# Performance work log

Measured on AMD Instinct MI355X. Metric: run time of the kernel, lower is better.

Reference implementation:

```python
import jax, jax.numpy as jnp
import numpy as np

D = 128

def setup_inputs() -> dict:
    key = jax.random.key(0)
    ks = jax.random.split(key, 9)
    B, Nq, Nk = 4, 4096, 4096
    Q = jax.random.normal(ks[0], (B, Nq, D), dtype=jnp.float32)
    K = jax.random.normal(ks[1], (B, Nk, D), dtype=jnp.float32)
    V = jax.random.normal(ks[2], (B, Nk, D), dtype=jnp.float32)
    s = 1.0 / np.sqrt(D)
    Wq = jax.random.normal(ks[3], (D, D), dtype=jnp.float32) * s
    Wk = jax.random.normal(ks[4], (D, D), dtype=jnp.float32) * s
    Wv = jax.random.normal(ks[5], (D, D), dtype=jnp.float32) * s
    bq = jax.random.normal(ks[6], (D,), dtype=jnp.float32) * s
    bk = jax.random.normal(ks[7], (D,), dtype=jnp.float32) * s
    bv = jax.random.normal(ks[8], (D,), dtype=jnp.float32) * s
    return {"Q": Q, "K": K, "V": V, "Wq": Wq, "bq": bq, "Wk": Wk, "bk": bk, "Wv": Wv, "bv": bv}

def reference(Q, K, V, Wq, bq, Wk, bk, Wv, bv):
    scale = jnp.asarray(D ** 0.5, dtype=Q.dtype)
    # torch Linear: x @ W.T + b
    q = jnp.einsum('bnd,ed->bne', Q, Wq) + bq
    k = jnp.einsum('bnd,ed->bne', K, Wk) + bk
    v = jnp.einsum('bnd,ed->bne', V, Wv) + bv
    scores = jnp.einsum('bqe,bke->bqk', q, k) / scale  # [B, Nq, Nk]
    attn = jax.nn.softmax(scores, axis=-1)
    return jnp.einsum('bqk,bke->bqe', attn, v)
```

## Files before the change

kernel.cpp:

```cpp
#include <hip/hip_runtime.h>
#include <math.h>

#define D 128
#define NSPLIT 4

typedef __bf16 v8bf __attribute__((ext_vector_type(8)));
typedef __bf16 v4bf __attribute__((ext_vector_type(4)));
typedef float v4f __attribute__((ext_vector_type(4)));

__device__ inline v8bf load_cvt8(const float* __restrict__ p) {
  const float4* p4 = (const float4*)p;
  float4 a = p4[0], b = p4[1];
  v8bf r;
  r[0] = (__bf16)a.x; r[1] = (__bf16)a.y; r[2] = (__bf16)a.z; r[3] = (__bf16)a.w;
  r[4] = (__bf16)b.x; r[5] = (__bf16)b.y; r[6] = (__bf16)b.z; r[7] = (__bf16)b.w;
  return r;
}

__device__ inline void async_copy16(const void* gsrc, void* ldst) {
  __builtin_amdgcn_global_load_lds(
      (const __attribute__((address_space(1))) void*)gsrc,
      (__attribute__((address_space(3))) void*)ldst, 16, 0, 0);
}

__global__ __launch_bounds__(256) void proj_all(
    const float* __restrict__ Q, const float* __restrict__ K,
    const float* __restrict__ V,
    const float* __restrict__ Wq, const float* __restrict__ bq,
    const float* __restrict__ Wk, const float* __restrict__ bk,
    const float* __restrict__ Wv, const float* __restrict__ bv,
    __bf16* __restrict__ qbf, __bf16* __restrict__ kbf,
    __bf16* __restrict__ vtbf, int Nk, float alpha)
{
  __shared__ __align__(16) __bf16 w_lds[128][136];

  const float* W    = (blockIdx.y == 0) ? Wq : (blockIdx.y == 1) ? Wk : Wv;
  const float* bias = (blockIdx.y == 0) ? bq : (blockIdx.y == 1) ? bk : bv;

  {
    const int tid = threadIdx.x;
    const int r = tid >> 1;
    const int h = (tid & 1) * 64;
    #pragma unroll
    for (int i = 0; i < 8; ++i) {
      v8bf v = load_cvt8(W + r * D + h + i * 8);
      *(v8bf*)&w_lds[r][h + i * 8] = v;
    }
  }
  __syncthreads();

  const int w = threadIdx.x >> 6, l = threadIdx.x & 63;
  const int l16 = l & 15, l4 = l >> 4;

  if (blockIdx.y < 2) {
    const float* X = (blockIdx.y == 0) ? Q : K;
    __bf16* Y      = (blockIdx.y == 0) ? qbf : kbf;
    const float a  = (blockIdx.y == 0) ? alpha : 1.0f;
    const size_t rbase = (size_t)blockIdx.x * 64 + w * 16;

    v4f acc[8];
    #pragma unroll
    for (int ct = 0; ct < 8; ++ct) acc[ct] = (v4f){0.f, 0.f, 0.f, 0.f};

    #pragma unroll
    for (int kk = 0; kk < 4; ++kk) {
      v8bf xv = load_cvt8(X + (rbase + l16) * D + kk * 32 + l4 * 8);
      #pragma unroll
      for (int ct = 0; ct < 8; ++ct) {
        v8bf wv = *(const v8bf*)&w_lds[ct * 16 + l16][kk * 32 + l4 * 8];
        acc[ct] = __builtin_amdgcn_mfma_f32_16x16x32_bf16(wv, xv, acc[ct], 0, 0, 0);
      }
    }
    const size_t qrow = rbase + l16;
    #pragma unroll
    for (int ct = 0; ct < 8; ++ct) {
      const int e0 = ct * 16 + l4 * 4;
      float4 b4 = *(const float4*)(bias + e0);
      v4bf o;
      o[0] = (__bf16)((acc[ct][0] + b4.x) * a);
      o[1] = (__bf16)((acc[ct][1] + b4.y) * a);
      o[2] = (__bf16)((acc[ct][2] + b4.z) * a);
      o[3] = (__bf16)((acc[ct][3] + b4.w) * a);
      *(v4bf*)(Y + qrow * D + e0) = o;
    }
  } else {
    const int bx = blockIdx.x;
    const int b = bx >> 6;
    const float* Xb = V + (size_t)b * Nk * D;
    __bf16* VTb = vtbf + (size_t)b * D * Nk;
    const int ebase = w * 32;
    const int nbase = (bx & 63) * 64;

    v4f acc[4][2];
    #pragma unroll
    for (int nt = 0; nt < 4; ++nt)
      #pragma unroll
      for (int et = 0; et < 2; ++et) acc[nt][et] = (v4f){0.f, 0.f, 0.f, 0.f};

    #pragma unroll
    for (int kk = 0; kk < 4; ++kk) {
      v8bf wv0 = *(const v8bf*)&w_lds[ebase + l16][kk * 32 + l4 * 8];
      v8bf wv1 = *(const v8bf*)&w_lds[ebase + 16 + l16][kk * 32 + l4 * 8];
      #pragma unroll
      for (int nt = 0; nt < 4; ++nt) {
        v8bf xv = load_cvt8(Xb + (size_t)(nbase + nt * 16 + l16) * D + kk * 32 + l4 * 8);
        acc[nt][0] = __builtin_amdgcn_mfma_f32_16x16x32_bf16(xv, wv0, acc[nt][0], 0, 0, 0);
        acc[nt][1] = __builtin_amdgcn_mfma_f32_16x16x32_bf16(xv, wv1, acc[nt][1], 0, 0, 0);
      }
    }
    #pragma unroll
    for (int et = 0; et < 2; ++et) {
      const int e = ebase + et * 16 + l16;
      const float bv2 = bias[e];
      __bf16* dst = VTb + (size_t)e * Nk + nbase;
      #pragma unroll
      for (int nt = 0; nt < 4; ++nt) {
        v4bf o;
        o[0] = (__bf16)(acc[nt][et][0] + bv2);
        o[1] = (__bf16)(acc[nt][et][1] + bv2);
        o[2] = (__bf16)(acc[nt][et][2] + bv2);
        o[3] = (__bf16)(acc[nt][et][3] + bv2);
        *(v4bf*)(dst + nt * 16 + l4 * 4) = o;
      }
    }
  }
}

__global__ __launch_bounds__(512, 2) void attn_fwd(
    const __bf16* __restrict__ Qb, const __bf16* __restrict__ Kb,
    const __bf16* __restrict__ VTb, float* __restrict__ Out,
    float2* __restrict__ ml, int Nq, int Nk, int NS, int B)
{
  const int nwg = gridDim.x;
  int id = blockIdx.x;
  id = (id & 7) * (nwg >> 3) + (id >> 3);
  const int nx = Nq >> 7;
  const int x = id % nx;
  const int s = (id / nx) % NS;
  const int b = id / (nx * NS);

  const int w = threadIdx.x >> 6, l = threadIdx.x & 63;
  const int l16 = l & 15, l4 = l >> 4;
  const int qbase = x * 128 + w * 16;
  const int chunk = Nk / NS;
  const int kvbeg = s * chunk;
  const int ntiles = chunk >> 6;

  const __bf16* q = Qb + ((size_t)b * Nq + qbase) * D;
  const char* kg0 = (const char*)(Kb + (size_t)b * Nk * D);
  const char* vg0 = (const char*)(VTb + (size_t)b * D * Nk);

  __shared__ __align__(16) char k_lds[2][16384];
  __shared__ __align__(16) char v_lds[2][16384];
  __shared__ __align__(16) char p_lds[8 * 2048];
  char* my_p = p_lds + w * 2048;

  const int NkB = Nk * 2;

  v8bf aq[4];
  #pragma unroll
  for (int kk = 0; kk < 4; ++kk)
    aq[kk] = *(const v8bf*)(q + l16 * D + kk * 32 + l4 * 8);

  v4f accO[8];
  #pragma unroll
  for (int ct = 0; ct < 8; ++ct) accO[ct] = (v4f){0.f, 0.f, 0.f, 0.f};
  float m[4], lsum[4];
  #pragma unroll
  for (int r = 0; r < 4; ++r) { m[r] = -1e30f; lsum[r] = 0.f; }

  auto stage = [&](int kv0, int buf) {
    const char* kg = kg0 + (size_t)kv0 * (D * 2);
    #pragma unroll
    for (int sweep = 0; sweep < 2; ++sweep) {
      const int flat = sweep * 8192 + w * 1024 + l * 16;
      const int row = flat >> 8;
      const int c = flat & 255;
      async_copy16(kg + ((row << 8) | (c ^ ((row & 7) << 4))),
                   &k_lds[buf][sweep * 8192 + w * 1024]);
    }
    const char* vg = vg0 + (size_t)kv0 * 2;
    #pragma unroll
    for (int sweep = 0; sweep < 2; ++sweep) {
      const int flat = sweep * 8192 + w * 1024 + l * 16;
      const int row = flat >> 7;
      const int c = flat & 127;
      async_copy16(vg + (size_t)row * NkB + (c ^ ((row & 7) << 4)),
                   &v_lds[buf][sweep * 8192 + w * 1024]);
    }
  };

  stage(kvbeg, 0);
  __syncthreads();

  for (int t = 0; t < ntiles; ++t) {
    const int cur = t & 1;
    if (t + 1 < ntiles) stage(kvbeg + (t + 1) * 64, cur ^ 1);

    v4f sc4[4];
    #pragma unroll
    for (int ct = 0; ct < 4; ++ct) sc4[ct] = (v4f){0.f, 0.f, 0.f, 0.f};
    #pragma unroll
    for (int ct = 0; ct < 4; ++ct) {
      const int krow = ct * 16 + l16;
      const int sw = (krow & 7) << 4;
      #pragma unroll
      for (int kk = 0; kk < 4; ++kk) {
        const int cb = kk * 64 + l4 * 16;
        v8bf bk = *(const v8bf*)(&k_lds[cur][krow * 256 + (cb ^ sw)]);
        sc4[ct] = __builtin_amdgcn_mfma_f32_16x16x32_bf16(aq[kk], bk, sc4[ct], 0, 0, 0);
      }
    }

    float lmax[4];
    float g = -1e30f;
    #pragma unroll
    for (int r = 0; r < 4; ++r) {
      lmax[r] = fmaxf(fmaxf(sc4[0][r], sc4[1][r]), fmaxf(sc4[2][r], sc4[3][r]));
      g = fmaxf(g, lmax[r] - m[r]);
    }
    if (__all(g <= 8.0f)) {
      #pragma unroll
      for (int r = 0; r < 4; ++r) {
        float rs = 0.f;
        #pragma unroll
        for (int ct = 0; ct < 4; ++ct) {
          float p = exp2f(sc4[ct][r] - m[r]);
          sc4[ct][r] = p;
          rs += p;
        }
        lsum[r] += rs;
      }
    } else {
      float scale[4];
      #pragma unroll
      for (int r = 0; r < 4; ++r) {
        float mx = lmax[r];
        #pragma unroll
        for (int off = 8; off; off >>= 1) mx = fmaxf(mx, __shfl_xor(mx, off, 64));
        float mn = fmaxf(m[r], mx);
        scale[r] = exp2f(m[r] - mn);
        m[r] = mn;
        float rs = 0.f;
        #pragma unroll
        for (int ct = 0; ct < 4; ++ct) {
          float p = exp2f(sc4[ct][r] - mn);
          sc4[ct][r] = p;
          rs += p;
        }
        lsum[r] = lsum[r] * scale[r] + rs;
      }
      #pragma unroll
      for (int ct = 0; ct < 8; ++ct)
        #pragma unroll
        for (int r = 0; r < 4; ++r) accO[ct][r] *= scale[r];
    }

    #pragma unroll
    for (int ct = 0; ct < 4; ++ct)
      #pragma unroll
      for (int r = 0; r < 4; ++r) {
        const int row = l4 * 4 + r;
        const int byte = row * 128 + ((ct * 32 + l16 * 2) ^ ((row & 7) << 4));
        *(__bf16*)(my_p + byte) = (__bf16)sc4[ct][r];
      }

    #pragma unroll
    for (int ks = 0; ks < 2; ++ks) {
      const int cbp = ks * 64 + l4 * 16;
      v8bf ap = *(const v8bf*)(my_p + l16 * 128 + (cbp ^ ((l16 & 7) << 4)));
      #pragma unroll
      for (int ct = 0; ct < 8; ++ct) {
        const int vrow = ct * 16 + l16;
        const int cb = ks * 64 + l4 * 16;
        v8bf bv = *(const v8bf*)(&v_lds[cur][vrow * 128 + (cb ^ ((vrow & 7) << 4))]);
        accO[ct] = __builtin_amdgcn_mfma_f32_16x16x32_bf16(ap, bv, accO[ct], 0, 0, 0);
      }
    }
    __syncthreads();
  }

  #pragma unroll
  for (int r = 0; r < 4; ++r) {
    float t2 = lsum[r];
    #pragma unroll
    for (int off = 8; off; off >>= 1) t2 += __shfl_xor(t2, off, 64);
    lsum[r] = t2;
  }

  float* outp = Out + (((size_t)s * B + b) * Nq + qbase) * D;
  if (NS == 1) {
    #pragma unroll
    for (int ct = 0; ct < 8; ++ct)
      #pragma unroll
      for (int r = 0; r < 4; ++r)
        outp[(size_t)(l4 * 4 + r) * D + ct * 16 + l16] = accO[ct][r] / lsum[r];
  } else {
    #pragma unroll
    for (int ct = 0; ct < 8; ++ct)
      #pragma unroll
      for (int r = 0; r < 4; ++r)
        outp[(size_t)(l4 * 4 + r) * D + ct * 16 + l16] = accO[ct][r];
    if (l16 == 0) {
      #pragma unroll
      for (int r = 0; r < 4; ++r) {
        size_t row = (size_t)b * Nq + qbase + l4 * 4 + r;
        ml[(size_t)s * B * Nq + row] = make_float2(m[r], lsum[r]);
      }
    }
  }
}

__global__ __launch_bounds__(256) void attn_combine(
    const float* __restrict__ Opart, const float2* __restrict__ ml,
    float* __restrict__ out, int NS, int rowsTotal)
{
  const int t = threadIdx.x;
  const size_t row = (size_t)blockIdx.x * 2 + (t >> 7);
  const int d = t & 127;

  float mv[NSPLIT], lv[NSPLIT];
  float M = -1e30f;
  #pragma unroll
  for (int s = 0; s < NSPLIT; ++s) {
    float2 x = ml[(size_t)s * rowsTotal + row];
    mv[s] = x.x; lv[s] = x.y;
    M = fmaxf(M, x.x);
  }
  float denom = 0.f, acc = 0.f;
  #pragma unroll
  for (int s = 0; s < NSPLIT; ++s) {
    float wgt = exp2f(mv[s] - M);
    denom += wgt * lv[s];
    acc += wgt * Opart[((size_t)s * rowsTotal + row) * D + d];
  }
  out[row * D + d] = acc / denom;
}

extern "C" void kernel_launch(void* const* d_in, const int* in_sizes, int n_in,
                              void* d_out, int out_size, void* d_ws, size_t ws_size,
                              hipStream_t stream) {
  const float* Q  = (const float*)d_in[0];
  const float* K  = (const float*)d_in[1];
  const float* V  = (const float*)d_in[2];
  const float* Wq = (const float*)d_in[3];
  const float* bq = (const float*)d_in[4];
  const float* Wk = (const float*)d_in[5];
  const float* bk = (const float*)d_in[6];
  const float* Wv = (const float*)d_in[7];
  const float* bv = (const float*)d_in[8];
  float* out = (float*)d_out;

  const int B = 4, Nq = 4096, Nk = 4096;
  const size_t nElems = (size_t)B * Nq * D;
  const size_t bfBytes = nElems * 2;

  char* ws = (char*)d_ws;
  __bf16* qbf  = (__bf16*)(ws);
  __bf16* kbf  = (__bf16*)(ws + bfBytes);
  __bf16* vtbf = (__bf16*)(ws + 2 * bfBytes);
  float*  Opart = (float*)(ws + 3 * bfBytes);
  float2* mlp   = (float2*)(ws + 3 * bfBytes + (size_t)NSPLIT * nElems * 4);

  const size_t needSplit = 3 * bfBytes + (size_t)NSPLIT * nElems * 4 +
                           (size_t)NSPLIT * B * Nq * 8;
  const int NS = (ws_size >= needSplit) ? NSPLIT : 1;

  const float alpha = 1.4426950408889634f / sqrtf((float)D);

  proj_all<<<dim3(B * Nq / 64, 3), 256, 0, stream>>>(
      Q, K, V, Wq, bq, Wk, bk, Wv, bv, qbf, kbf, vtbf, Nk, alpha);

  const int nx = Nq / 128;
  if (NS == 1) {
    attn_fwd<<<dim3(nx * B), 512, 0, stream>>>(
        qbf, kbf, vtbf, out, nullptr, Nq, Nk, 1, B);
  } else {
    attn_fwd<<<dim3(nx * NS * B), 512, 0, stream>>>(
        qbf, kbf, vtbf, Opart, mlp, Nq, Nk, NS, B);
    attn_combine<<<dim3(B * Nq / 2), 256, 0, stream>>>(
        Opart, mlp, out, NS, B * Nq);
  }
}
```

Baseline: 181.4 us.

## Process 32 query rows per wave with 4 waves per block

Each wave now handles two 16-row query sub-tiles instead of one, so every K and V fragment read from LDS feeds two MFMAs. Blocks shrink from 8 waves to 4, with each wave issuing twice as many async copies for staging. This halves LDS read traffic per MFMA, at the cost of roughly doubled accumulator and score register use per wave, which may lower occupancy and cuts the number of waves available to hide latency.

```diff
diff --git a/kernel.cpp b/kernel.cpp
--- a/kernel.cpp
+++ b/kernel.cpp
@@ -126,7 +126,7 @@
   }
 }
 
-__global__ __launch_bounds__(512, 2) void attn_fwd(
+__global__ __launch_bounds__(256, 2) void attn_fwd(
     const __bf16* __restrict__ Qb, const __bf16* __restrict__ Kb,
     const __bf16* __restrict__ VTb, float* __restrict__ Out,
     float2* __restrict__ ml, int Nq, int Nk, int NS, int B)
@@ -141,7 +141,7 @@
 
   const int w = threadIdx.x >> 6, l = threadIdx.x & 63;
   const int l16 = l & 15, l4 = l >> 4;
-  const int qbase = x * 128 + w * 16;
+  const int qbase = x * 128 + w * 32;
   const int chunk = Nk / NS;
   const int kvbeg = s * chunk;
   const int ntiles = chunk >> 6;
@@ -152,41 +152,47 @@
 
   __shared__ __align__(16) char k_lds[2][16384];
   __shared__ __align__(16) char v_lds[2][16384];
-  __shared__ __align__(16) char p_lds[8 * 2048];
-  char* my_p = p_lds + w * 2048;
+  __shared__ __align__(16) char p_lds[4 * 4096];
+  char* my_p = p_lds + w * 4096;
 
   const int NkB = Nk * 2;
 
-  v8bf aq[4];
-  #pragma unroll
-  for (int kk = 0; kk < 4; ++kk)
-    aq[kk] = *(const v8bf*)(q + l16 * D + kk * 32 + l4 * 8);
-
-  v4f accO[8];
-  #pragma unroll
-  for (int ct = 0; ct < 8; ++ct) accO[ct] = (v4f){0.f, 0.f, 0.f, 0.f};
-  float m[4], lsum[4];
-  #pragma unroll
-  for (int r = 0; r < 4; ++r) { m[r] = -1e30f; lsum[r] = 0.f; }
+  v8bf aq[2][4];
+  #pragma unroll
+  for (int qs = 0; qs < 2; ++qs)
+    #pragma unroll
+    for (int kk = 0; kk < 4; ++kk)
+      aq[qs][kk] = *(const v8bf*)(q + (qs * 16 + l16) * D + kk * 32 + l4 * 8);
+
+  v4f accO[2][8];
+  #pragma unroll
+  for (int qs = 0; qs < 2; ++qs)
+    #pragma unroll
+    for (int ct = 0; ct < 8; ++ct) accO[qs][ct] = (v4f){0.f, 0.f, 0.f, 0.f};
+  float m[2][4], lsum[2][4];
+  #pragma unroll
+  for (int qs = 0; qs < 2; ++qs)
+    #pragma unroll
+    for (int r = 0; r < 4; ++r) { m[qs][r] = -1e30f; lsum[qs][r] = 0.f; }
 
   auto stage = [&](int kv0, int buf) {
     const char* kg = kg0 + (size_t)kv0 * (D * 2);
     #pragma unroll
-    for (int sweep = 0; sweep < 2; ++sweep) {
-      const int flat = sweep * 8192 + w * 1024 + l * 16;
+    for (int sweep = 0; sweep < 4; ++sweep) {
+      const int flat = sweep * 4096 + w * 1024 + l * 16;
       const int row = flat >> 8;
       const int c = flat & 255;
       async_copy16(kg + ((row << 8) | (c ^ ((row & 7) << 4))),
-                   &k_lds[buf][sweep * 8192 + w * 1024]);
+                   &k_lds[buf][sweep * 4096 + w * 1024]);
     }
     const char* vg = vg0 + (size_t)kv0 * 2;
     #pragma unroll
-    for (int sweep = 0; sweep < 2; ++sweep) {
-      const int flat = sweep * 8192 + w * 1024 + l * 16;
+    for (int sweep = 0; sweep < 4; ++sweep) {
+      const int flat = sweep * 4096 + w * 1024 + l * 16;
       const int row = flat >> 7;
       const int c = flat & 127;
       async_copy16(vg + (size_t)row * NkB + (c ^ ((row & 7) << 4)),
-                   &v_lds[buf][sweep * 8192 + w * 1024]);
+                   &v_lds[buf][sweep * 4096 + w * 1024]);
     }
   };
 
@@ -197,9 +203,11 @@
     const int cur = t & 1;
     if (t + 1 < ntiles) stage(kvbeg + (t + 1) * 64, cur ^ 1);
 
-    v4f sc4[4];
-    #pragma unroll
-    for (int ct = 0; ct < 4; ++ct) sc4[ct] = (v4f){0.f, 0.f, 0.f, 0.f};
+    v4f sc4[2][4];
+    #pragma unroll
+    for (int qs = 0; qs < 2; ++qs)
+      #pragma unroll
+      for (int ct = 0; ct < 4; ++ct) sc4[qs][ct] = (v4f){0.f, 0.f, 0.f, 0.f};
     #pragma unroll
     for (int ct = 0; ct < 4; ++ct) {
       const int krow = ct * 16 + l16;
@@ -208,105 +216,122 @@
       for (int kk = 0; kk < 4; ++kk) {
         const int cb = kk * 64 + l4 * 16;
         v8bf bk = *(const v8bf*)(&k_lds[cur][krow * 256 + (cb ^ sw)]);
-        sc4[ct] = __builtin_amdgcn_mfma_f32_16x16x32_bf16(aq[kk], bk, sc4[ct], 0, 0, 0);
-      }
-    }
-
-    float lmax[4];
-    float g = -1e30f;
-    #pragma unroll
-    for (int r = 0; r < 4; ++r) {
-      lmax[r] = fmaxf(fmaxf(sc4[0][r], sc4[1][r]), fmaxf(sc4[2][r], sc4[3][r]));
-      g = fmaxf(g, lmax[r] - m[r]);
-    }
-    if (__all(g <= 8.0f)) {
+        sc4[0][ct] = __builtin_amdgcn_mfma_f32_16x16x32_bf16(aq[0][kk], bk, sc4[0][ct], 0, 0, 0);
+        sc4[1][ct] = __builtin_amdgcn_mfma_f32_16x16x32_bf16(aq[1][kk], bk, sc4[1][ct], 0, 0, 0);
+      }
+    }
+
+    #pragma unroll
+    for (int qs = 0; qs < 2; ++qs) {
+      float lmax[4];
+      float g = -1e30f;
       #pragma unroll
       for (int r = 0; r < 4; ++r) {
-        float rs = 0.f;
-        #pragma unroll
-        for (int ct = 0; ct < 4; ++ct) {
-          float p = exp2f(sc4[ct][r] - m[r]);
-          sc4[ct][r] = p;
-          rs += p;
+        lmax[r] = fmaxf(fmaxf(sc4[qs][0][r], sc4[qs][1][r]),
+                        fmaxf(sc4[qs][2][r], sc4[qs][3][r]));
+        g = fmaxf(g, lmax[r] - m[qs][r]);
+      }
+      if (__all(g <= 8.0f)) {
+        #pragma unroll
+        for (int r = 0; r < 4; ++r) {
+          float rs = 0.f;
+          #pragma unroll
+          for (int ct = 0; ct < 4; ++ct) {
+            float p = exp2f(sc4[qs][ct][r] - m[qs][r]);
+            sc4[qs][ct][r] = p;
+            rs += p;
+          }
+          lsum[qs][r] += rs;
         }
-        lsum[r] += rs;
-      }
-    } else {
-      float scale[4];
-      #pragma unroll
-      for (int r = 0; r < 4; ++r) {
-        float mx = lmax[r];
-        #pragma unroll
-        for (int off = 8; off; off >>= 1) mx = fmaxf(mx, __shfl_xor(mx, off, 64));
-        float mn = fmaxf(m[r], mx);
-        scale[r] = exp2f(m[r] - mn);
-        m[r] = mn;
-        float rs = 0.f;
-        #pragma unroll
-        for (int ct = 0; ct < 4; ++ct) {
-          float p = exp2f(sc4[ct][r] - mn);
-          sc4[ct][r] = p;
-          rs += p;
+      } else {
+        float scale[4];
+        #pragma unroll
+        for (int r = 0; r < 4; ++r) {
+          float mx = lmax[r];
+          #pragma unroll
+          for (int off = 8; off; off >>= 1) mx = fmaxf(mx, __shfl_xor(mx, off, 64));
+          float mn = fmaxf(m[qs][r], mx);
+          scale[r] = exp2f(m[qs][r] - mn);
+          m[qs][r] = mn;
+          float rs = 0.f;
+          #pragma unroll
+          for (int ct = 0; ct < 4; ++ct) {
+            float p = exp2f(sc4[qs][ct][r] - mn);
+            sc4[qs][ct][r] = p;
+            rs += p;
+          }
+          lsum[qs][r] = lsum[qs][r] * scale[r] + rs;
         }
-        lsum[r] = lsum[r] * scale[r] + rs;
-      }
-      #pragma unroll
-      for (int ct = 0; ct < 8; ++ct)
-        #pragma unroll
-        for (int r = 0; r < 4; ++r) accO[ct][r] *= scale[r];
-    }
-
-    #pragma unroll
-    for (int ct = 0; ct < 4; ++ct)
-      #pragma unroll
-      for (int r = 0; r < 4; ++r) {
-        const int row = l4 * 4 + r;
-        const int byte = row * 128 + ((ct * 32 + l16 * 2) ^ ((row & 7) << 4));
-        *(__bf16*)(my_p + byte) = (__bf16)sc4[ct][r];
-      }
+        #pragma unroll
+        for (int ct = 0; ct < 8; ++ct)
+          #pragma unroll
+          for (int r = 0; r < 4; ++r) accO[qs][ct][r] *= scale[r];
+      }
+
+      #pragma unroll
+      for (int ct = 0; ct < 4; ++ct)
+        #pragma unroll
+        for (int r = 0; r < 4; ++r) {
+          const int row = l4 * 4 + r;
+          const int byte = qs * 2048 + row * 128 +
+                           ((ct * 32 + l16 * 2) ^ ((row & 7) << 4));
+          *(__bf16*)(my_p + byte) = (__bf16)sc4[qs][ct][r];
+        }
+    }
 
     #pragma unroll
     for (int ks = 0; ks < 2; ++ks) {
       const int cbp = ks * 64 + l4 * 16;
-      v8bf ap = *(const v8bf*)(my_p + l16 * 128 + (cbp ^ ((l16 & 7) << 4)));
+      v8bf ap0 = *(const v8bf*)(my_p + l16 * 128 + (cbp ^ ((l16 & 7) << 4)));
+      v8bf ap1 = *(const v8bf*)(my_p + 2048 + l16 * 128 + (cbp ^ ((l16 & 7) << 4)));
       #pragma unroll
       for (int ct = 0; ct < 8; ++ct) {
         const int vrow = ct * 16 + l16;
         const int cb = ks * 64 + l4 * 16;
         v8bf bv = *(const v8bf*)(&v_lds[cur][vrow * 128 + (cb ^ ((vrow & 7) << 4))]);
-        accO[ct] = __builtin_amdgcn_mfma_f32_16x16x32_bf16(ap, bv, accO[ct], 0, 0, 0);
+        accO[0][ct] = __builtin_amdgcn_mfma_f32_16x16x32_bf16(ap0, bv, accO[0][ct], 0, 0, 0);
+        accO[1][ct] = __builtin_amdgcn_mfma_f32_16x16x32_bf16(ap1, bv, accO[1][ct], 0, 0, 0);
       }
     }
     __syncthreads();
   }
 
   #pragma unroll
-  for (int r = 0; r < 4; ++r) {
-    float t2 = lsum[r];
-    #pragma unroll
-    for (int off = 8; off; off >>= 1) t2 += __shfl_xor(t2, off, 64);
-    lsum[r] = t2;
-  }
+  for (int qs = 0; qs < 2; ++qs)
+    #pragma unroll
+    for (int r = 0; r < 4; ++r) {
+      float t2 = lsum[qs][r];
+      #pragma unroll
+      for (int off = 8; off; off >>= 1) t2 += __shfl_xor(t2, off, 64);
+      lsum[qs][r] = t2;
+    }
 
   float* outp = Out + (((size_t)s * B + b) * Nq + qbase) * D;
   if (NS == 1) {
     #pragma unroll
-    for (int ct = 0; ct < 8; ++ct)
-      #pragma unroll
-      for (int r = 0; r < 4; ++r)
-        outp[(size_t)(l4 * 4 + r) * D + ct * 16 + l16] = accO[ct][r] / lsum[r];
+    for (int qs = 0; qs < 2; ++qs)
+      #pragma unroll
+      for (int ct = 0; ct < 8; ++ct)
+        #pragma unroll
+        for (int r = 0; r < 4; ++r)
+          outp[(size_t)(qs * 16 + l4 * 4 + r) * D + ct * 16 + l16] =
+              accO[qs][ct][r] / lsum[qs][r];
   } else {
     #pragma unroll
-    for (int ct = 0; ct < 8; ++ct)
-      #pragma unroll
-      for (int r = 0; r < 4; ++r)
-        outp[(size_t)(l4 * 4 + r) * D + ct * 16 + l16] = accO[ct][r];
+    for (int qs = 0; qs < 2; ++qs)
+      #pragma unroll
+      for (int ct = 0; ct < 8; ++ct)
+        #pragma unroll
+        for (int r = 0; r < 4; ++r)
+          outp[(size_t)(qs * 16 + l4 * 4 + r) * D + ct * 16 + l16] = accO[qs][ct][r];
     if (l16 == 0) {
       #pragma unroll
-      for (int r = 0; r < 4; ++r) {
-        size_t row = (size_t)b * Nq + qbase + l4 * 4 + r;
-        ml[(size_t)s * B * Nq + row] = make_float2(m[r], lsum[r]);
-      }
+      for (int qs = 0; qs < 2; ++qs)
+        #pragma unroll
+        for (int r = 0; r < 4; ++r) {
+          size_t row = (size_t)b * Nq + qbase + qs * 16 + l4 * 4 + r;
+          ml[(size_t)s * B * Nq + row] = make_float2(m[qs][r], lsum[qs][r]);
+        }
     }
   }
 }
@@ -373,10 +398,10 @@
 
   const int nx = Nq / 128;
   if (NS == 1) {
-    attn_fwd<<<dim3(nx * B), 512, 0, stream>>>(
+    attn_fwd<<<dim3(nx * B), 256, 0, stream>>>(
         qbf, kbf, vtbf, out, nullptr, Nq, Nk, 1, B);
   } else {
-    attn_fwd<<<dim3(nx * NS * B), 512, 0, stream>>>(
+    attn_fwd<<<dim3(nx * NS * B), 256, 0, stream>>>(
         qbf, kbf, vtbf, Opart, mlp, Nq, Nk, NS, B);
     attn_combine<<<dim3(B * Nq / 2), 256, 0, stream>>>(
         Opart, mlp, out, NS, B * Nq);
```

Result: faster. 168.4 us (-7.1%).
